# Optimization experiments

Measured on AMD Instinct MI355X. Metric: run time of the kernel, lower is better.

The kernel has to match this reference:

```python
import jax, jax.numpy as jnp
import numpy as np

B, S, D, H, F = 4, 2048, 256, 8, 2  # batch, seq, input_size, heads, mlp factor
EPS = 1e-5


def _ln(x, g, b):
    m = jnp.mean(x, axis=-1, keepdims=True)
    v = jnp.var(x, axis=-1, keepdims=True)
    return (x - m) / jnp.sqrt(v + EPS) * g + b


def setup_inputs() -> dict:
    key = jax.random.key(0)
    ks = jax.random.split(key, 12)
    s = 1.0 / np.sqrt(D)
    return {
        "X":  jax.random.normal(ks[0], (B, S, D), jnp.float32),
        # Wide attention: each of H heads has full [D,D] Q/K/V projections (no bias)
        "Wq": jax.random.uniform(ks[1], (H, D, D), jnp.float32, -s, s),
        "Wk": jax.random.uniform(ks[2], (H, D, D), jnp.float32, -s, s),
        "Wv": jax.random.uniform(ks[3], (H, D, D), jnp.float32, -s, s),
        "Wz": jax.random.uniform(ks[4], (H * D, D), jnp.float32, -1.0 / np.sqrt(H * D), 1.0 / np.sqrt(H * D)),
        "bz": jnp.zeros((D,), jnp.float32),
        "W1": jax.random.uniform(ks[5], (D, F * D), jnp.float32, -s, s),
        "b1": jnp.zeros((F * D,), jnp.float32),
        "W2": jax.random.uniform(ks[6], (F * D, D), jnp.float32, -1.0 / np.sqrt(F * D), 1.0 / np.sqrt(F * D)),
        "b2": jnp.zeros((D,), jnp.float32),
        "g1": jnp.ones((D,), jnp.float32),
        "be1": jnp.zeros((D,), jnp.float32),
        "g2": jnp.ones((D,), jnp.float32),
        "be2": jnp.zeros((D,), jnp.float32),
    }


def reference(X, Wq, Wk, Wv, Wz, bz, W1, b1, W2, b2, g1, be1, g2, be2):
    scale = D ** (-0.25)  # applied to both q and k as in the source
    q = jnp.einsum('bsd,hde->hbse', X, Wq) * scale   # [H,B,S,D]
    k = jnp.einsum('btd,hde->hbte', X, Wk) * scale
    v = jnp.einsum('btd,hde->hbte', X, Wv)
    attn = jax.nn.softmax(jnp.einsum('hbse,hbte->hbst', q, k), axis=-1)  # [H,B,S,S]
    zh = jnp.einsum('hbst,hbte->hbse', attn, v)       # [H,B,S,D]
    # concat heads along feature dim (head order matters for Wz)
    zcat = jnp.transpose(zh, (1, 2, 0, 3)).reshape(B, S, H * D)
    z = zcat @ Wz + bz
    z = _ln(z + X, g1, be1)                            # dropout p=0 -> identity
    z_ff = jnp.maximum(z @ W1 + b1, 0.0) @ W2 + b2
    z = _ln(z_ff + z, g2, be2)
    attn_mean = jnp.mean(attn, axis=0)                 # [B,S,S]
    return z, attn_mean
```

## Files before the change

### kernel.cpp

```cpp
#include <hip/hip_runtime.h>
#include <cstdint>
#include <cstddef>

#define B_  4
#define S_  2048
#define D_  256
#define H_  8
#define FD_ 512
#define N_  (B_*S_)
#define HD_ (H_*D_)
#define EPS 1e-5f

typedef __attribute__((ext_vector_type(8))) short bf16x8;
typedef __attribute__((ext_vector_type(8))) unsigned short u16x8;
typedef __attribute__((ext_vector_type(4))) float f32x4;

__device__ __forceinline__ unsigned short f2bf(float f) {
  union { float f; unsigned u; } x; x.f = f;
  unsigned u = x.u;
  return (unsigned short)((u + 0x7FFFu + ((u >> 16) & 1u)) >> 16);
}
__device__ __forceinline__ float bf2f(unsigned short h) {
  union { unsigned u; float f; } x; x.u = ((unsigned)h) << 16; return x.f;
}

__device__ __forceinline__ void glds16(const void* gptr, void* ldsptr) {
  __builtin_amdgcn_global_load_lds(
      (__attribute__((address_space(1))) void*)gptr,
      (__attribute__((address_space(3))) void*)ldsptr,
      16, 0, 0);
}

__device__ __forceinline__ int sw32(int row, int u) {
  return (row*32 + ((u & 24) | ((u & 7) ^ (row & 7)))) * 8;
}
__device__ __forceinline__ int sw16(int row, int u) {
  return (row*16 + ((u & 8) | ((u & 7) ^ (row & 7)))) * 8;
}

__global__ __launch_bounds__(256) void prep_fat_kernel(
    const float* __restrict__ X, unsigned short* __restrict__ Xb,
    const float* __restrict__ Wq, const float* __restrict__ Wk,
    const float* __restrict__ Wv, unsigned short* __restrict__ Wt,
    const float* __restrict__ Wz, unsigned short* __restrict__ Wzt,
    const float* __restrict__ W1, unsigned short* __restrict__ W1t,
    const float* __restrict__ W2, unsigned short* __restrict__ W2t)
{
  __shared__ float tile[64][65];
  const int tid = threadIdx.x;
  const int bid = blockIdx.x;

  if (bid < 1024) {
    const size_t i8 = ((size_t)bid * 256 + tid) * 8;
    float4 a = *(const float4*)&X[i8];
    float4 b = *(const float4*)&X[i8 + 4];
    u16x8 o;
    o[0]=f2bf(a.x); o[1]=f2bf(a.y); o[2]=f2bf(a.z); o[3]=f2bf(a.w);
    o[4]=f2bf(b.x); o[5]=f2bf(b.y); o[6]=f2bf(b.z); o[7]=f2bf(b.w);
    *(u16x8*)&Xb[i8] = o;
    return;
  }

  const float* src;
  unsigned short* dst_base;
  int R, C;
  float scale = 1.0f;
  int d0, e0;
  bool is_prepw = false;
  int wsel = 0;

  if (bid < 1408) {
    int idx = bid - 1024;
    d0 = (idx & 3) * 64;
    e0 = ((idx >> 2) & 3) * 64;
    wsel = idx >> 4;
    if (wsel < 8)       { src = Wq + (size_t)wsel*D_*D_;      scale = 0.25f; }
    else if (wsel < 16) { src = Wk + (size_t)(wsel-8)*D_*D_;  scale = 0.25f; }
    else                { src = Wv + (size_t)(wsel-16)*D_*D_; scale = 1.0f;  }
    R = D_; C = D_;
    dst_base = Wt;
    is_prepw = true;
  } else if (bid < 1536) {
    int idx = bid - 1408;
    d0 = (idx & 31) * 64;
    e0 = (idx >> 5) * 64;
    src = Wz; dst_base = Wzt; R = HD_; C = D_;
  } else if (bid < 1568) {
    int idx = bid - 1536;
    d0 = (idx & 3) * 64;
    e0 = (idx >> 2) * 64;
    src = W1; dst_base = W1t; R = D_; C = FD_;
  } else {
    int idx = bid - 1568;
    d0 = (idx & 7) * 64;
    e0 = (idx >> 3) * 64;
    src = W2; dst_base = W2t; R = FD_; C = D_;
  }

  {
    int r = tid >> 2, c16 = (tid & 3) * 16;
    const float* s = src + (size_t)(d0 + r)*C + e0 + c16;
    #pragma unroll
    for (int u = 0; u < 4; ++u) *(float4*)&tile[r][c16 + u*4] = *(const float4*)(s + u*4);
  }
  __syncthreads();
  {
    int cr = tid >> 2, rc = (tid & 3) * 16;
    u16x8 o0, o1;
    #pragma unroll
    for (int j = 0; j < 8; ++j) {
      o0[j] = f2bf(tile[rc + j][cr] * scale);
      o1[j] = f2bf(tile[rc + 8 + j][cr] * scale);
    }
    unsigned short* d;
    if (is_prepw)
      d = dst_base + ((size_t)wsel*D_ + e0 + cr)*D_ + d0 + rc;
    else
      d = dst_base + (size_t)(e0 + cr)*R + d0 + rc;
    *(u16x8*)(d)     = o0;
    *(u16x8*)(d + 8) = o1;
  }
}

__global__ __launch_bounds__(256) void qkv_kernel(
    const unsigned short* __restrict__ Xb, const unsigned short* __restrict__ Wt,
    unsigned short* __restrict__ q, unsigned short* __restrict__ k,
    unsigned short* __restrict__ vT)
{
  __shared__ unsigned short Xt[64*32*8];
  __shared__ unsigned short Wtile[64*32*8];
  const int tid = threadIdx.x;
  const int w4 = tid >> 6, lane = tid & 63;
  const int c = lane & 15, qd = lane >> 4;
  const int n0 = blockIdx.x * 64;
  const int e0 = blockIdx.y * 64;
  const int w  = blockIdx.z;

  {
    const char* xg = (const char*)Xb + (size_t)n0*512;
    const char* wg = (const char*)Wt + ((size_t)w*D_ + e0)*512;
    #pragma unroll
    for (int i = 0; i < 8; ++i) {
      int g = w4*8 + i;
      int r = 2*g + (lane >> 5);
      int su = lane & 31;
      int u = (su & 24) | ((su & 7) ^ (r & 7));
      glds16(xg + (size_t)r*512 + u*16, &Xt[g*512]);
      glds16(wg + (size_t)r*512 + u*16, &Wtile[g*512]);
    }
  }
  __syncthreads();

  f32x4 sc[4];
  #pragma unroll
  for (int nc = 0; nc < 4; ++nc) sc[nc] = (f32x4){0.f,0.f,0.f,0.f};
  #pragma unroll
  for (int ks = 0; ks < 8; ++ks) {
    bf16x8 xa = *(const bf16x8*)&Xt[sw32(16*w4 + c, ks*4 + qd)];
    #pragma unroll
    for (int nc = 0; nc < 4; ++nc) {
      bf16x8 bf = *(const bf16x8*)&Wtile[sw32(nc*16 + c, ks*4 + qd)];
      sc[nc] = __builtin_amdgcn_mfma_f32_16x16x32_bf16(xa, bf, sc[nc], 0, 0, 0);
    }
  }

  if (w < 16) {
    unsigned short* obase = (w < 8) ? (q + (size_t)w*N_*D_)
                                    : (k + (size_t)(w-8)*N_*D_);
    #pragma unroll
    for (int nc = 0; nc < 4; ++nc)
      #pragma unroll
      for (int r = 0; r < 4; ++r)
        obase[(size_t)(n0 + 16*w4 + qd*4 + r)*D_ + e0 + nc*16 + c] = f2bf(sc[nc][r]);
  } else {
    const int h = w - 16;
    const int b = n0 >> 11;
    const int t0 = n0 & (S_ - 1);
    unsigned short (*tile)[72] = (unsigned short (*)[72])Xt;
    __syncthreads();
    #pragma unroll
    for (int nc = 0; nc < 4; ++nc)
      #pragma unroll
      for (int r = 0; r < 4; ++r)
        tile[16*w4 + qd*4 + r][nc*16 + c] = f2bf(sc[nc][r]);
    __syncthreads();
    {
      int er = tid >> 2, tt = (tid & 3) * 16;
      u16x8 o0, o1;
      #pragma unroll
      for (int j = 0; j < 8; ++j) { o0[j] = tile[tt+j][er]; o1[j] = tile[tt+8+j][er]; }
      unsigned short* dst = vT + ((size_t)(h*4 + b)*D_ + e0 + er)*S_ + t0 + tt;
      *(u16x8*)(dst)     = o0;
      *(u16x8*)(dst + 8) = o1;
    }
  }
}

__global__ __launch_bounds__(256, 2) void attn_ol_kernel(
    const unsigned short* __restrict__ qb, const unsigned short* __restrict__ kb,
    const unsigned short* __restrict__ vT, unsigned short* __restrict__ zcatb,
    float* __restrict__ Lws)
{
  __shared__ unsigned short Kt[2][32*32*8];
  __shared__ unsigned short Vt[2][16*544];
  const int tid = threadIdx.x;
  const int w = tid >> 6, lane = tid & 63;
  const int c = lane & 15, qd = lane >> 4;
  const int wg = blockIdx.x;
  const int xcd = wg & 7;
  const int slot = wg >> 3;
  const int j = slot & 15;
  const int gg = slot >> 4;
  const int g = gg*8 + xcd;
  const int h = g >> 2, b = g & 3;
  const int s0 = j * 128;

  const size_t qkbase = (size_t)h*N_*D_ + (size_t)b*S_*D_;

  bf16x8 qa[2][8];
  #pragma unroll
  for (int mi = 0; mi < 2; ++mi) {
    const unsigned short* qrow = qb + qkbase + (size_t)(s0 + 32*w + 16*mi + c)*D_ + qd*8;
    #pragma unroll
    for (int ks = 0; ks < 8; ++ks) qa[mi][ks] = *(const bf16x8*)(qrow + ks*32);
  }

  f32x4 o[2][16];
  #pragma unroll
  for (int mi = 0; mi < 2; ++mi)
    #pragma unroll
    for (int i = 0; i < 16; ++i) o[mi][i] = (f32x4){0.f,0.f,0.f,0.f};
  float Lp[2] = {0.f, 0.f};

  const char* kB = (const char*)(kb + qkbase);
  const char* vB = (const char*)(vT + (size_t)(h*4 + b)*D_*S_);

  #define STAGE_OL(kt_, bi_)                                                   \
    {                                                                          \
      _Pragma("unroll")                                                        \
      for (int i = 0; i < 4; ++i) {                                            \
        int gq = w*4 + i;                                                      \
        int r = 2*gq + (lane >> 5);                                            \
        int Lg = ((r >> 2) & 3)*8 + (r >> 4)*4 + (r & 3);                      \
        int su = lane & 31;                                                    \
        int u = (su & 24) | ((su & 7) ^ (r & 7));                              \
        glds16(kB + ((size_t)(kt_)*32 + Lg)*512 + u*16, &Kt[bi_][gq*512]);     \
      }                                                                        \
      _Pragma("unroll")                                                        \
      for (int i = 0; i < 4; ++i) {                                            \
        int gq = w*4 + i;                                                      \
        int e = gq*16 + (lane >> 2);                                           \
        int qv = (lane & 3) ^ ((lane >> 3) & 3);                               \
        glds16(vB + (size_t)e*4096 + (size_t)(kt_)*64 + qv*16, &Vt[bi_][gq*544]);\
      }                                                                        \
    }

  STAGE_OL(0, 0);

  for (int kt = 0; kt < 64; ++kt) {
    const int bi = kt & 1;
    __syncthreads();
    if (kt + 1 < 64) STAGE_OL(kt + 1, bi ^ 1);

    f32x4 sc[2][2];
    #pragma unroll
    for (int mi = 0; mi < 2; ++mi)
      #pragma unroll
      for (int nc = 0; nc < 2; ++nc) sc[mi][nc] = (f32x4){0.f,0.f,0.f,0.f};
    #pragma unroll
    for (int ks = 0; ks < 8; ++ks) {
      bf16x8 kf0 = *(const bf16x8*)&Kt[bi][sw32(c,      ks*4 + qd)];
      bf16x8 kf1 = *(const bf16x8*)&Kt[bi][sw32(16 + c, ks*4 + qd)];
      #pragma unroll
      for (int mi = 0; mi < 2; ++mi) {
        sc[mi][0] = __builtin_amdgcn_mfma_f32_16x16x32_bf16(kf0, qa[mi][ks], sc[mi][0], 0, 0, 0);
        sc[mi][1] = __builtin_amdgcn_mfma_f32_16x16x32_bf16(kf1, qa[mi][ks], sc[mi][1], 0, 0, 0);
      }
    }
    bf16x8 pa[2];
    #pragma unroll
    for (int mi = 0; mi < 2; ++mi) {
      float ex[2][4];
      #pragma unroll
      for (int nc = 0; nc < 2; ++nc)
        #pragma unroll
        for (int r = 0; r < 4; ++r) {
          float p = __expf(sc[mi][nc][r]);
          ex[nc][r] = p;
          Lp[mi] += p;
        }
      union { unsigned u[4]; bf16x8 v; } cv;
      asm("v_cvt_pk_bf16_f32 %0, %1, %2" : "=v"(cv.u[0]) : "v"(ex[0][0]), "v"(ex[0][1]));
      asm("v_cvt_pk_bf16_f32 %0, %1, %2" : "=v"(cv.u[1]) : "v"(ex[0][2]), "v"(ex[0][3]));
      asm("v_cvt_pk_bf16_f32 %0, %1, %2" : "=v"(cv.u[2]) : "v"(ex[1][0]), "v"(ex[1][1]));
      asm("v_cvt_pk_bf16_f32 %0, %1, %2" : "=v"(cv.u[3]) : "v"(ex[1][2]), "v"(ex[1][3]));
      pa[mi] = cv.v;
    }
    #pragma unroll
    for (int ec = 0; ec < 16; ++ec) {
      bf16x8 vf = *(const bf16x8*)&Vt[bi][ec*544 + c*32 + (qd ^ ((c >> 1) & 3))*8];
      o[0][ec] = __builtin_amdgcn_mfma_f32_16x16x32_bf16(pa[0], vf, o[0][ec], 0, 0, 0);
      o[1][ec] = __builtin_amdgcn_mfma_f32_16x16x32_bf16(pa[1], vf, o[1][ec], 0, 0, 0);
    }
  }

  #pragma unroll
  for (int mi = 0; mi < 2; ++mi) {
    float L = Lp[mi];
    L += __shfl_xor(L, 16);
    L += __shfl_xor(L, 32);
    if (qd == 0)
      Lws[(size_t)h*N_ + b*S_ + s0 + 32*w + 16*mi + c] = L;
    float il[4];
    #pragma unroll
    for (int r = 0; r < 4; ++r)
      il[r] = 1.0f / __shfl(L, (lane & 48) | (qd*4 + r));
    #pragma unroll
    for (int ec = 0; ec < 16; ++ec)
      #pragma unroll
      for (int r = 0; r < 4; ++r)
        zcatb[(size_t)(b*S_ + s0 + 32*w + 16*mi + qd*4 + r)*HD_ + h*D_ + ec*16 + c] =
            f2bf(o[mi][ec][r] * il[r]);
  }
  #undef STAGE_OL
}

__global__ __launch_bounds__(256) void wz_ln1_kernel(
    const unsigned short* __restrict__ zcatb, const unsigned short* __restrict__ Wzt,
    const float* __restrict__ bz, const float* __restrict__ X,
    const float* __restrict__ g1, const float* __restrict__ be1,
    unsigned short* __restrict__ z1b)
{
  __shared__ unsigned short At[32*16*8];
  __shared__ unsigned short Wt2[256*16*8];
  __shared__ float redS[2][32], redQ[2][32];
  const int tid = threadIdx.x;
  const int w4 = tid >> 6, lane = tid & 63;
  const int c = lane & 15, qd = lane >> 4;
  const int n0 = blockIdx.x * 32;
  const int msub = w4 & 1, ehalf = w4 >> 1;

  f32x4 acc[8];
  #pragma unroll
  for (int nc = 0; nc < 8; ++nc) acc[nc] = (f32x4){0.f,0.f,0.f,0.f};

  for (int kc = 0; kc < 16; ++kc) {
    {
      const char* ab = (const char*)zcatb + (size_t)n0*4096 + (size_t)kc*256;
      #pragma unroll
      for (int i = 0; i < 2; ++i) {
        int g = w4*2 + i;
        int r = g*4 + (lane >> 4);
        int su = lane & 15;
        int u = (su & 8) | ((su & 7) ^ (r & 7));
        glds16(ab + (size_t)r*4096 + u*16, &At[g*512]);
      }
      const char* wb = (const char*)Wzt + (size_t)kc*256;
      #pragma unroll
      for (int i = 0; i < 16; ++i) {
        int g = w4*16 + i;
        int e = g*4 + (lane >> 4);
        int su = lane & 15;
        int u = (su & 8) | ((su & 7) ^ (e & 7));
        glds16(wb + (size_t)e*4096 + u*16, &Wt2[g*512]);
      }
    }
    __syncthreads();
    #pragma unroll
    for (int ks = 0; ks < 4; ++ks) {
      bf16x8 a = *(const bf16x8*)&At[sw16(msub*16 + c, ks*4 + qd)];
      #pragma unroll
      for (int nc = 0; nc < 8; ++nc) {
        bf16x8 bv = *(const bf16x8*)&Wt2[sw16(ehalf*128 + nc*16 + c, ks*4 + qd)];
        acc[nc] = __builtin_amdgcn_mfma_f32_16x16x32_bf16(a, bv, acc[nc], 0, 0, 0);
      }
    }
    __syncthreads();
  }

  float vals[8][4];
  float sum_[4] = {0.f,0.f,0.f,0.f}, sq_[4] = {0.f,0.f,0.f,0.f};
  #pragma unroll
  for (int nc = 0; nc < 8; ++nc) {
    int e = ehalf*128 + nc*16 + c;
    #pragma unroll
    for (int r = 0; r < 4; ++r) {
      int n = n0 + msub*16 + qd*4 + r;
      float v = acc[nc][r] + bz[e] + X[(size_t)n*D_ + e];
      vals[nc][r] = v;
      sum_[r] += v; sq_[r] += v*v;
    }
  }
  #pragma unroll
  for (int off = 1; off < 16; off <<= 1) {
    #pragma unroll
    for (int r = 0; r < 4; ++r) {
      sum_[r] += __shfl_xor(sum_[r], off);
      sq_[r]  += __shfl_xor(sq_[r],  off);
    }
  }
  if (c == 0) {
    #pragma unroll
    for (int r = 0; r < 4; ++r) {
      redS[ehalf][msub*16 + qd*4 + r] = sum_[r];
      redQ[ehalf][msub*16 + qd*4 + r] = sq_[r];
    }
  }
  __syncthreads();
  #pragma unroll
  for (int r = 0; r < 4; ++r) {
    int lr = msub*16 + qd*4 + r;
    float Sv = redS[0][lr] + redS[1][lr];
    float Qv = redQ[0][lr] + redQ[1][lr];
    float mean = Sv * (1.0f/D_);
    float var  = Qv * (1.0f/D_) - mean*mean;
    float rstd = rsqrtf(var + EPS);
    int n = n0 + lr;
    #pragma unroll
    for (int nc = 0; nc < 8; ++nc) {
      int e = ehalf*128 + nc*16 + c;
      z1b[(size_t)n*D_ + e] = f2bf((vals[nc][r] - mean)*rstd*g1[e] + be1[e]);
    }
  }
}

__global__ __launch_bounds__(256, 2) void attn_mean_mlp1_kernel(
    const unsigned short* __restrict__ qb, const unsigned short* __restrict__ kb,
    const float* __restrict__ Lws, float* __restrict__ out_attn,
    const unsigned short* __restrict__ z1b, const unsigned short* __restrict__ W1t,
    const float* __restrict__ b1, unsigned short* __restrict__ hbuf)
{
  __shared__ __align__(16) char smem[65536];
  const int tid = threadIdx.x;
  const int w = tid >> 6, lane = tid & 63;
  const int c = lane & 15, qd = lane >> 4;
  const int bid = blockIdx.x;

  if (bid < 2048) {
    unsigned short (*Kt)[64*32*8] = (unsigned short (*)[64*32*8])smem;
    const int xcd = bid & 7;
    const int slot = bid >> 3;
    const int j = slot & 15;
    const int ggg = slot >> 4;
    const int g = ggg*8 + xcd;
    const int b = g >> 5;
    const int t0 = (g & 31) * 64;
    const int s0 = j * 128;

    float am[2][4][4] = {};

    #define STAGE_AM(h_, bi_)                                                  \
      {                                                                        \
        const char* kB = (const char*)(kb + (size_t)(h_)*N_*D_ + (size_t)b*S_*D_);\
        _Pragma("unroll")                                                      \
        for (int i = 0; i < 8; ++i) {                                          \
          int gq = w*8 + i;                                                    \
          int r = 2*gq + (lane >> 5);                                          \
          int su = lane & 31;                                                  \
          int u = (su & 24) | ((su & 7) ^ (r & 7));                            \
          glds16(kB + ((size_t)t0 + r)*512 + u*16, &Kt[bi_][gq*512]);          \
        }                                                                      \
      }

    STAGE_AM(0, 0);

    bf16x8 qa[2][8];
    #pragma unroll
    for (int mi = 0; mi < 2; ++mi) {
      const unsigned short* qrow = qb + (size_t)b*S_*D_ + (size_t)(s0 + 32*w + 16*mi + c)*D_ + qd*8;
      #pragma unroll
      for (int ks = 0; ks < 8; ++ks) qa[mi][ks] = *(const bf16x8*)(qrow + ks*32);
    }

    for (int h = 0; h < 8; ++h) {
      const int bi = h & 1;
      __syncthreads();
      if (h + 1 < 8) STAGE_AM(h + 1, bi ^ 1);

      float il[2][4];
      #pragma unroll
      for (int mi = 0; mi < 2; ++mi)
        #pragma unroll
        for (int r = 0; r < 4; ++r)
          il[mi][r] = 0.125f / Lws[(size_t)h*N_ + b*S_ + s0 + 32*w + 16*mi + qd*4 + r];

      bf16x8 qn[2][8];
      if (h + 1 < 8) {
        const size_t basen = (size_t)(h+1)*N_*D_ + (size_t)b*S_*D_;
        #pragma unroll
        for (int mi = 0; mi < 2; ++mi) {
          const unsigned short* qrow = qb + basen + (size_t)(s0 + 32*w + 16*mi + c)*D_ + qd*8;
          #pragma unroll
          for (int ks = 0; ks < 8; ++ks) qn[mi][ks] = *(const bf16x8*)(qrow + ks*32);
        }
      }

      f32x4 sc[2][4];
      #pragma unroll
      for (int mi = 0; mi < 2; ++mi)
        #pragma unroll
        for (int nc = 0; nc < 4; ++nc) sc[mi][nc] = (f32x4){0.f,0.f,0.f,0.f};
      #pragma unroll
      for (int ks = 0; ks < 8; ++ks) {
        #pragma unroll
        for (int nc = 0; nc < 4; ++nc) {
          bf16x8 kf = *(const bf16x8*)&Kt[bi][sw32(nc*16 + c, ks*4 + qd)];
          sc[0][nc] = __builtin_amdgcn_mfma_f32_16x16x32_bf16(qa[0][ks], kf, sc[0][nc], 0, 0, 0);
          sc[1][nc] = __builtin_amdgcn_mfma_f32_16x16x32_bf16(qa[1][ks], kf, sc[1][nc], 0, 0, 0);
        }
      }
      #pragma unroll
      for (int mi = 0; mi < 2; ++mi)
        #pragma unroll
        for (int nc = 0; nc < 4; ++nc)
          #pragma unroll
          for (int r = 0; r < 4; ++r)
            am[mi][nc][r] += __expf(sc[mi][nc][r]) * il[mi][r];

      if (h + 1 < 8) {
        #pragma unroll
        for (int mi = 0; mi < 2; ++mi)
          #pragma unroll
          for (int ks = 0; ks < 8; ++ks) qa[mi][ks] = qn[mi][ks];
      }
    }
    #pragma unroll
    for (int mi = 0; mi < 2; ++mi)
      #pragma unroll
      for (int nc = 0; nc < 4; ++nc)
        #pragma unroll
        for (int r = 0; r < 4; ++r)
          out_attn[(size_t)(b*S_ + s0 + 32*w + 16*mi + qd*4 + r)*S_ + t0 + nc*16 + c] =
              am[mi][nc][r];
    #undef STAGE_AM
  } else {
    unsigned short* At = (unsigned short*)smem;
    unsigned short* Bt = (unsigned short*)(smem + 32768);
    const int idx = bid - 2048;
    const int n0 = (idx & 127) * 64;
    const int f0 = (idx >> 7) * 64;
    const int w4 = w;

    {
      const char* ag = (const char*)z1b + (size_t)n0*512;
      const char* bg = (const char*)W1t + (size_t)f0*512;
      #pragma unroll
      for (int i = 0; i < 8; ++i) {
        int g = w4*8 + i;
        int r = 2*g + (lane >> 5);
        int su = lane & 31;
        int u = (su & 24) | ((su & 7) ^ (r & 7));
        glds16(ag + (size_t)r*512 + u*16, &At[g*512]);
        glds16(bg + (size_t)r*512 + u*16, &Bt[g*512]);
      }
    }
    __syncthreads();

    f32x4 sc[4];
    #pragma unroll
    for (int nc = 0; nc < 4; ++nc) sc[nc] = (f32x4){0.f,0.f,0.f,0.f};
    #pragma unroll
    for (int ks = 0; ks < 8; ++ks) {
      bf16x8 xa = *(const bf16x8*)&At[sw32(16*w4 + c, ks*4 + qd)];
      #pragma unroll
      for (int nc = 0; nc < 4; ++nc) {
        bf16x8 bf = *(const bf16x8*)&Bt[sw32(nc*16 + c, ks*4 + qd)];
        sc[nc] = __builtin_amdgcn_mfma_f32_16x16x32_bf16(xa, bf, sc[nc], 0, 0, 0);
      }
    }
    #pragma unroll
    for (int nc = 0; nc < 4; ++nc) {
      int f = f0 + nc*16 + c;
      float bias = b1[f];
      #pragma unroll
      for (int r = 0; r < 4; ++r)
        hbuf[(size_t)(n0 + 16*w4 + qd*4 + r)*FD_ + f] = f2bf(fmaxf(sc[nc][r] + bias, 0.f));
    }
  }
}

__global__ __launch_bounds__(256) void mlp2_kernel(
    const unsigned short* __restrict__ hbuf, const unsigned short* __restrict__ W2t,
    const float* __restrict__ b2, const unsigned short* __restrict__ z1b,
    const float* __restrict__ g2, const float* __restrict__ be2,
    float* __restrict__ out)
{
  __shared__ unsigned short At[32*16*8];
  __shared__ unsigned short Wt2[256*16*8];
  __shared__ float redS[2][32], redQ[2][32];
  const int tid = threadIdx.x;
  const int w4 = tid >> 6, lane = tid & 63;
  const int c = lane & 15, qd = lane >> 4;
  const int n0 = blockIdx.x * 32;
  const int msub = w4 & 1, ehalf = w4 >> 1;

  f32x4 acc[8];
  #pragma unroll
  for (int nc = 0; nc < 8; ++nc) acc[nc] = (f32x4){0.f,0.f,0.f,0.f};

  for (int kc = 0; kc < 4; ++kc) {
    {
      const char* ab = (const char*)hbuf + (size_t)n0*1024 + (size_t)kc*256;
      #pragma unroll
      for (int i = 0; i < 2; ++i) {
        int g = w4*2 + i;
        int r = g*4 + (lane >> 4);
        int su = lane & 15;
        int u = (su & 8) | ((su & 7) ^ (r & 7));
        glds16(ab + (size_t)r*1024 + u*16, &At[g*512]);
      }
      const char* wb = (const char*)W2t + (size_t)kc*256;
      #pragma unroll
      for (int i = 0; i < 16; ++i) {
        int g = w4*16 + i;
        int e = g*4 + (lane >> 4);
        int su = lane & 15;
        int u = (su & 8) | ((su & 7) ^ (e & 7));
        glds16(wb + (size_t)e*1024 + u*16, &Wt2[g*512]);
      }
    }
    __syncthreads();
    #pragma unroll
    for (int ks = 0; ks < 4; ++ks) {
      bf16x8 a = *(const bf16x8*)&At[sw16(msub*16 + c, ks*4 + qd)];
      #pragma unroll
      for (int nc = 0; nc < 8; ++nc) {
        bf16x8 bv = *(const bf16x8*)&Wt2[sw16(ehalf*128 + nc*16 + c, ks*4 + qd)];
        acc[nc] = __builtin_amdgcn_mfma_f32_16x16x32_bf16(a, bv, acc[nc], 0, 0, 0);
      }
    }
    __syncthreads();
  }

  float vals[8][4];
  float sum_[4] = {0.f,0.f,0.f,0.f}, sq_[4] = {0.f,0.f,0.f,0.f};
  #pragma unroll
  for (int nc = 0; nc < 8; ++nc) {
    int e = ehalf*128 + nc*16 + c;
    #pragma unroll
    for (int r = 0; r < 4; ++r) {
      int n = n0 + msub*16 + qd*4 + r;
      float v = acc[nc][r] + b2[e] + bf2f(z1b[(size_t)n*D_ + e]);
      vals[nc][r] = v;
      sum_[r] += v; sq_[r] += v*v;
    }
  }
  #pragma unroll
  for (int off = 1; off < 16; off <<= 1) {
    #pragma unroll
    for (int r = 0; r < 4; ++r) {
      sum_[r] += __shfl_xor(sum_[r], off);
      sq_[r]  += __shfl_xor(sq_[r],  off);
    }
  }
  if (c == 0) {
    #pragma unroll
    for (int r = 0; r < 4; ++r) {
      redS[ehalf][msub*16 + qd*4 + r] = sum_[r];
      redQ[ehalf][msub*16 + qd*4 + r] = sq_[r];
    }
  }
  __syncthreads();
  #pragma unroll
  for (int r = 0; r < 4; ++r) {
    int lr = msub*16 + qd*4 + r;
    float Sv = redS[0][lr] + redS[1][lr];
    float Qv = redQ[0][lr] + redQ[1][lr];
    float mean = Sv * (1.0f/D_);
    float var  = Qv * (1.0f/D_) - mean*mean;
    float rstd = rsqrtf(var + EPS);
    int n = n0 + lr;
    #pragma unroll
    for (int nc = 0; nc < 8; ++nc) {
      int e = ehalf*128 + nc*16 + c;
      out[(size_t)n*D_ + e] = (vals[nc][r] - mean)*rstd*g2[e] + be2[e];
    }
  }
}

extern "C" void kernel_launch(void* const* d_in, const int* in_sizes, int n_in,
                              void* d_out, int out_size, void* d_ws, size_t ws_size,
                              hipStream_t stream)
{
  (void)in_sizes; (void)n_in; (void)out_size; (void)ws_size;
  const float* X   = (const float*)d_in[0];
  const float* Wq  = (const float*)d_in[1];
  const float* Wk  = (const float*)d_in[2];
  const float* Wv  = (const float*)d_in[3];
  const float* Wz  = (const float*)d_in[4];
  const float* bz  = (const float*)d_in[5];
  const float* W1  = (const float*)d_in[6];
  const float* b1  = (const float*)d_in[7];
  const float* W2  = (const float*)d_in[8];
  const float* b2  = (const float*)d_in[9];
  const float* g1  = (const float*)d_in[10];
  const float* be1 = (const float*)d_in[11];
  const float* g2  = (const float*)d_in[12];
  const float* be2 = (const float*)d_in[13];

  char* p = (char*)d_ws;
  unsigned short* Xbb  = (unsigned short*)p; p += (size_t)N_*D_*2;
  unsigned short* Wtb  = (unsigned short*)p; p += (size_t)24*D_*D_*2;
  unsigned short* Wztb = (unsigned short*)p; p += (size_t)D_*HD_*2;
  unsigned short* W1tb = (unsigned short*)p; p += (size_t)FD_*D_*2;
  unsigned short* W2tb = (unsigned short*)p; p += (size_t)D_*FD_*2;
  unsigned short* qbuf = (unsigned short*)p; p += (size_t)H_*N_*D_*2;
  unsigned short* kbuf = (unsigned short*)p; p += (size_t)H_*N_*D_*2;
  unsigned short* vbuf = (unsigned short*)p; p += (size_t)H_*N_*D_*2;
  unsigned short* vTb  = (unsigned short*)p; p += (size_t)H_*N_*D_*2;
  float* Lws   = (float*)p; p += (size_t)H_*N_*4;
  unsigned short* zcatb = (unsigned short*)p; p += (size_t)N_*HD_*2;
  unsigned short* z1b   = (unsigned short*)p; p += (size_t)N_*D_*2;
  unsigned short* hbuf  = (unsigned short*)p;
  (void)vbuf;

  float* out_z    = (float*)d_out;
  float* out_attn = out_z + (size_t)N_*D_;

  prep_fat_kernel<<<1600, 256, 0, stream>>>(
      X, Xbb, Wq, Wk, Wv, Wtb, Wz, Wztb, W1, W1tb, W2, W2tb);

  dim3 gA(N_/64, D_/64, 24);
  qkv_kernel<<<gA, 256, 0, stream>>>(Xbb, Wtb, qbuf, kbuf, vTb);

  attn_ol_kernel<<<512, 256, 0, stream>>>(qbuf, kbuf, vTb, zcatb, Lws);

  wz_ln1_kernel<<<N_/32, 256, 0, stream>>>(zcatb, Wztb, bz, X, g1, be1, z1b);

  attn_mean_mlp1_kernel<<<3072, 256, 0, stream>>>(
      qbuf, kbuf, Lws, out_attn, z1b, W1tb, b1, hbuf);

  mlp2_kernel<<<N_/32, 256, 0, stream>>>(hbuf, W2tb, b2, z1b, g2, be2, out_z);
}
```

Baseline: 504.7 us.

## Split attention-mean work across two fused kernels to overlap Wz+LN1 and MLP1

The attention-mean computation is split into two halves over query blocks. The first half now runs in the same launch as the Wz projection plus LayerNorm1, and the second half in the same launch as the MLP1 GEMM. This is meant to hide the small, low-occupancy Wz/LN1 kernel behind independent attention-mean work and balance the two launches. The Wz/LN1 branch now uses a larger shared allocation (about 74KB) under launch bounds of 2 blocks per CU, which can reduce occupancy for the attention-mean blocks in that launch.

```diff
diff --git a/kernel.cpp b/kernel.cpp
--- a/kernel.cpp
+++ b/kernel.cpp
@@ -325,123 +325,27 @@
   #undef STAGE_OL
 }
 
-__global__ __launch_bounds__(256) void wz_ln1_kernel(
+#define FATSMEM (73728 + 512)
+__global__ __launch_bounds__(256, 2) void fat_a_kernel(
+    const unsigned short* __restrict__ qb, const unsigned short* __restrict__ kb,
+    const float* __restrict__ Lws, float* __restrict__ out_attn,
     const unsigned short* __restrict__ zcatb, const unsigned short* __restrict__ Wzt,
     const float* __restrict__ bz, const float* __restrict__ X,
     const float* __restrict__ g1, const float* __restrict__ be1,
     unsigned short* __restrict__ z1b)
 {
-  __shared__ unsigned short At[32*16*8];
-  __shared__ unsigned short Wt2[256*16*8];
-  __shared__ float redS[2][32], redQ[2][32];
-  const int tid = threadIdx.x;
-  const int w4 = tid >> 6, lane = tid & 63;
-  const int c = lane & 15, qd = lane >> 4;
-  const int n0 = blockIdx.x * 32;
-  const int msub = w4 & 1, ehalf = w4 >> 1;
-
-  f32x4 acc[8];
-  #pragma unroll
-  for (int nc = 0; nc < 8; ++nc) acc[nc] = (f32x4){0.f,0.f,0.f,0.f};
-
-  for (int kc = 0; kc < 16; ++kc) {
-    {
-      const char* ab = (const char*)zcatb + (size_t)n0*4096 + (size_t)kc*256;
-      #pragma unroll
-      for (int i = 0; i < 2; ++i) {
-        int g = w4*2 + i;
-        int r = g*4 + (lane >> 4);
-        int su = lane & 15;
-        int u = (su & 8) | ((su & 7) ^ (r & 7));
-        glds16(ab + (size_t)r*4096 + u*16, &At[g*512]);
-      }
-      const char* wb = (const char*)Wzt + (size_t)kc*256;
-      #pragma unroll
-      for (int i = 0; i < 16; ++i) {
-        int g = w4*16 + i;
-        int e = g*4 + (lane >> 4);
-        int su = lane & 15;
-        int u = (su & 8) | ((su & 7) ^ (e & 7));
-        glds16(wb + (size_t)e*4096 + u*16, &Wt2[g*512]);
-      }
-    }
-    __syncthreads();
-    #pragma unroll
-    for (int ks = 0; ks < 4; ++ks) {
-      bf16x8 a = *(const bf16x8*)&At[sw16(msub*16 + c, ks*4 + qd)];
-      #pragma unroll
-      for (int nc = 0; nc < 8; ++nc) {
-        bf16x8 bv = *(const bf16x8*)&Wt2[sw16(ehalf*128 + nc*16 + c, ks*4 + qd)];
-        acc[nc] = __builtin_amdgcn_mfma_f32_16x16x32_bf16(a, bv, acc[nc], 0, 0, 0);
-      }
-    }
-    __syncthreads();
-  }
-
-  float vals[8][4];
-  float sum_[4] = {0.f,0.f,0.f,0.f}, sq_[4] = {0.f,0.f,0.f,0.f};
-  #pragma unroll
-  for (int nc = 0; nc < 8; ++nc) {
-    int e = ehalf*128 + nc*16 + c;
-    #pragma unroll
-    for (int r = 0; r < 4; ++r) {
-      int n = n0 + msub*16 + qd*4 + r;
-      float v = acc[nc][r] + bz[e] + X[(size_t)n*D_ + e];
-      vals[nc][r] = v;
-      sum_[r] += v; sq_[r] += v*v;
-    }
-  }
-  #pragma unroll
-  for (int off = 1; off < 16; off <<= 1) {
-    #pragma unroll
-    for (int r = 0; r < 4; ++r) {
-      sum_[r] += __shfl_xor(sum_[r], off);
-      sq_[r]  += __shfl_xor(sq_[r],  off);
-    }
-  }
-  if (c == 0) {
-    #pragma unroll
-    for (int r = 0; r < 4; ++r) {
-      redS[ehalf][msub*16 + qd*4 + r] = sum_[r];
-      redQ[ehalf][msub*16 + qd*4 + r] = sq_[r];
-    }
-  }
-  __syncthreads();
-  #pragma unroll
-  for (int r = 0; r < 4; ++r) {
-    int lr = msub*16 + qd*4 + r;
-    float Sv = redS[0][lr] + redS[1][lr];
-    float Qv = redQ[0][lr] + redQ[1][lr];
-    float mean = Sv * (1.0f/D_);
-    float var  = Qv * (1.0f/D_) - mean*mean;
-    float rstd = rsqrtf(var + EPS);
-    int n = n0 + lr;
-    #pragma unroll
-    for (int nc = 0; nc < 8; ++nc) {
-      int e = ehalf*128 + nc*16 + c;
-      z1b[(size_t)n*D_ + e] = f2bf((vals[nc][r] - mean)*rstd*g1[e] + be1[e]);
-    }
-  }
-}
-
-__global__ __launch_bounds__(256, 2) void attn_mean_mlp1_kernel(
-    const unsigned short* __restrict__ qb, const unsigned short* __restrict__ kb,
-    const float* __restrict__ Lws, float* __restrict__ out_attn,
-    const unsigned short* __restrict__ z1b, const unsigned short* __restrict__ W1t,
-    const float* __restrict__ b1, unsigned short* __restrict__ hbuf)
-{
-  __shared__ __align__(16) char smem[65536];
+  __shared__ __align__(16) char smem[FATSMEM];
   const int tid = threadIdx.x;
   const int w = tid >> 6, lane = tid & 63;
   const int c = lane & 15, qd = lane >> 4;
   const int bid = blockIdx.x;
 
-  if (bid < 2048) {
+  if (bid < 1024) {
     unsigned short (*Kt)[64*32*8] = (unsigned short (*)[64*32*8])smem;
     const int xcd = bid & 7;
     const int slot = bid >> 3;
-    const int j = slot & 15;
-    const int ggg = slot >> 4;
+    const int j = slot & 7;
+    const int ggg = slot >> 3;
     const int g = ggg*8 + xcd;
     const int b = g >> 5;
     const int t0 = (g & 31) * 64;
@@ -534,9 +438,212 @@
               am[mi][nc][r];
     #undef STAGE_AM
   } else {
+    unsigned short* At  = (unsigned short*)smem;
+    unsigned short* Wt2 = (unsigned short*)(smem + 8192);
+    float (*redS)[32] = (float (*)[32])(smem + 73728);
+    float (*redQ)[32] = (float (*)[32])(smem + 73728 + 256);
+    const int n0 = (bid - 1024) * 32;
+    const int w4 = w;
+    const int msub = w4 & 1, ehalf = w4 >> 1;
+
+    f32x4 acc[8];
+    #pragma unroll
+    for (int nc = 0; nc < 8; ++nc) acc[nc] = (f32x4){0.f,0.f,0.f,0.f};
+
+    for (int kc = 0; kc < 16; ++kc) {
+      {
+        const char* ab = (const char*)zcatb + (size_t)n0*4096 + (size_t)kc*256;
+        #pragma unroll
+        for (int i = 0; i < 2; ++i) {
+          int g = w4*2 + i;
+          int r = g*4 + (lane >> 4);
+          int su = lane & 15;
+          int u = (su & 8) | ((su & 7) ^ (r & 7));
+          glds16(ab + (size_t)r*4096 + u*16, &At[g*512]);
+        }
+        const char* wb = (const char*)Wzt + (size_t)kc*256;
+        #pragma unroll
+        for (int i = 0; i < 16; ++i) {
+          int g = w4*16 + i;
+          int e = g*4 + (lane >> 4);
+          int su = lane & 15;
+          int u = (su & 8) | ((su & 7) ^ (e & 7));
+          glds16(wb + (size_t)e*4096 + u*16, &Wt2[g*512]);
+        }
+      }
+      __syncthreads();
+      #pragma unroll
+      for (int ks = 0; ks < 4; ++ks) {
+        bf16x8 a = *(const bf16x8*)&At[sw16(msub*16 + c, ks*4 + qd)];
+        #pragma unroll
+        for (int nc = 0; nc < 8; ++nc) {
+          bf16x8 bv = *(const bf16x8*)&Wt2[sw16(ehalf*128 + nc*16 + c, ks*4 + qd)];
+          acc[nc] = __builtin_amdgcn_mfma_f32_16x16x32_bf16(a, bv, acc[nc], 0, 0, 0);
+        }
+      }
+      __syncthreads();
+    }
+
+    float vals[8][4];
+    float sum_[4] = {0.f,0.f,0.f,0.f}, sq_[4] = {0.f,0.f,0.f,0.f};
+    #pragma unroll
+    for (int nc = 0; nc < 8; ++nc) {
+      int e = ehalf*128 + nc*16 + c;
+      #pragma unroll
+      for (int r = 0; r < 4; ++r) {
+        int n = n0 + msub*16 + qd*4 + r;
+        float v = acc[nc][r] + bz[e] + X[(size_t)n*D_ + e];
+        vals[nc][r] = v;
+        sum_[r] += v; sq_[r] += v*v;
+      }
+    }
+    #pragma unroll
+    for (int off = 1; off < 16; off <<= 1) {
+      #pragma unroll
+      for (int r = 0; r < 4; ++r) {
+        sum_[r] += __shfl_xor(sum_[r], off);
+        sq_[r]  += __shfl_xor(sq_[r],  off);
+      }
+    }
+    if (c == 0) {
+      #pragma unroll
+      for (int r = 0; r < 4; ++r) {
+        redS[ehalf][msub*16 + qd*4 + r] = sum_[r];
+        redQ[ehalf][msub*16 + qd*4 + r] = sq_[r];
+      }
+    }
+    __syncthreads();
+    #pragma unroll
+    for (int r = 0; r < 4; ++r) {
+      int lr = msub*16 + qd*4 + r;
+      float Sv = redS[0][lr] + redS[1][lr];
+      float Qv = redQ[0][lr] + redQ[1][lr];
+      float mean = Sv * (1.0f/D_);
+      float var  = Qv * (1.0f/D_) - mean*mean;
+      float rstd = rsqrtf(var + EPS);
+      int n = n0 + lr;
+      #pragma unroll
+      for (int nc = 0; nc < 8; ++nc) {
+        int e = ehalf*128 + nc*16 + c;
+        z1b[(size_t)n*D_ + e] = f2bf((vals[nc][r] - mean)*rstd*g1[e] + be1[e]);
+      }
+    }
+  }
+}
+
+__global__ __launch_bounds__(256, 2) void fat_b_kernel(
+    const unsigned short* __restrict__ qb, const unsigned short* __restrict__ kb,
+    const float* __restrict__ Lws, float* __restrict__ out_attn,
+    const unsigned short* __restrict__ z1b, const unsigned short* __restrict__ W1t,
+    const float* __restrict__ b1, unsigned short* __restrict__ hbuf)
+{
+  __shared__ __align__(16) char smem[65536];
+  const int tid = threadIdx.x;
+  const int w = tid >> 6, lane = tid & 63;
+  const int c = lane & 15, qd = lane >> 4;
+  const int bid = blockIdx.x;
+
+  if (bid < 1024) {
+    unsigned short (*Kt)[64*32*8] = (unsigned short (*)[64*32*8])smem;
+    const int xcd = bid & 7;
+    const int slot = bid >> 3;
+    const int j = 8 + (slot & 7);
+    const int ggg = slot >> 3;
+    const int g = ggg*8 + xcd;
+    const int b = g >> 5;
+    const int t0 = (g & 31) * 64;
+    const int s0 = j * 128;
+
+    float am[2][4][4] = {};
+
+    #define STAGE_AM(h_, bi_)                                                  \
+      {                                                                        \
+        const char* kB = (const char*)(kb + (size_t)(h_)*N_*D_ + (size_t)b*S_*D_);\
+        _Pragma("unroll")                                                      \
+        for (int i = 0; i < 8; ++i) {                                          \
+          int gq = w*8 + i;                                                    \
+          int r = 2*gq + (lane >> 5);                                          \
+          int su = lane & 31;                                                  \
+          int u = (su & 24) | ((su & 7) ^ (r & 7));                            \
+          glds16(kB + ((size_t)t0 + r)*512 + u*16, &Kt[bi_][gq*512]);          \
+        }                                                                      \
+      }
+
+    STAGE_AM(0, 0);
+
+    bf16x8 qa[2][8];
+    #pragma unroll
+    for (int mi = 0; mi < 2; ++mi) {
+      const unsigned short* qrow = qb + (size_t)b*S_*D_ + (size_t)(s0 + 32*w + 16*mi + c)*D_ + qd*8;
+      #pragma unroll
+      for (int ks = 0; ks < 8; ++ks) qa[mi][ks] = *(const bf16x8*)(qrow + ks*32);
+    }
+
+    for (int h = 0; h < 8; ++h) {
+      const int bi = h & 1;
+      __syncthreads();
+      if (h + 1 < 8) STAGE_AM(h + 1, bi ^ 1);
+
+      float il[2][4];
+      #pragma unroll
+      for (int mi = 0; mi < 2; ++mi)
+        #pragma unroll
+        for (int r = 0; r < 4; ++r)
+          il[mi][r] = 0.125f / Lws[(size_t)h*N_ + b*S_ + s0 + 32*w + 16*mi + qd*4 + r];
+
+      bf16x8 qn[2][8];
+      if (h + 1 < 8) {
+        const size_t basen = (size_t)(h+1)*N_*D_ + (size_t)b*S_*D_;
+        #pragma unroll
+        for (int mi = 0; mi < 2; ++mi) {
+          const unsigned short* qrow = qb + basen + (size_t)(s0 + 32*w + 16*mi + c)*D_ + qd*8;
+          #pragma unroll
+          for (int ks = 0; ks < 8; ++ks) qn[mi][ks] = *(const bf16x8*)(qrow + ks*32);
+        }
+      }
+
+      f32x4 sc[2][4];
+      #pragma unroll
+      for (int mi = 0; mi < 2; ++mi)
+        #pragma unroll
+        for (int nc = 0; nc < 4; ++nc) sc[mi][nc] = (f32x4){0.f,0.f,0.f,0.f};
+      #pragma unroll
+      for (int ks = 0; ks < 8; ++ks) {
+        #pragma unroll
+        for (int nc = 0; nc < 4; ++nc) {
+          bf16x8 kf = *(const bf16x8*)&Kt[bi][sw32(nc*16 + c, ks*4 + qd)];
+          sc[0][nc] = __builtin_amdgcn_mfma_f32_16x16x32_bf16(qa[0][ks], kf, sc[0][nc], 0, 0, 0);
+          sc[1][nc] = __builtin_amdgcn_mfma_f32_16x16x32_bf16(qa[1][ks], kf, sc[1][nc], 0, 0, 0);
+        }
+      }
+      #pragma unroll
+      for (int mi = 0; mi < 2; ++mi)
+        #pragma unroll
+        for (int nc = 0; nc < 4; ++nc)
+          #pragma unroll
+          for (int r = 0; r < 4; ++r)
+            am[mi][nc][r] += __expf(sc[mi][nc][r]) * il[mi][r];
+
+      if (h + 1 < 8) {
+        #pragma unroll
+        for (int mi = 0; mi < 2; ++mi)
+          #pragma unroll
+          for (int ks = 0; ks < 8; ++ks) qa[mi][ks] = qn[mi][ks];
+      }
+    }
+    #pragma unroll
+    for (int mi = 0; mi < 2; ++mi)
+      #pragma unroll
+      for (int nc = 0; nc < 4; ++nc)
+        #pragma unroll
+        for (int r = 0; r < 4; ++r)
+          out_attn[(size_t)(b*S_ + s0 + 32*w + 16*mi + qd*4 + r)*S_ + t0 + nc*16 + c] =
+              am[mi][nc][r];
+    #undef STAGE_AM
+  } else {
     unsigned short* At = (unsigned short*)smem;
     unsigned short* Bt = (unsigned short*)(smem + 32768);
-    const int idx = bid - 2048;
+    const int idx = bid - 1024;
     const int n0 = (idx & 127) * 64;
     const int f0 = (idx >> 7) * 64;
     const int w4 = w;
@@ -725,9 +832,10 @@
 
   attn_ol_kernel<<<512, 256, 0, stream>>>(qbuf, kbuf, vTb, zcatb, Lws);
 
-  wz_ln1_kernel<<<N_/32, 256, 0, stream>>>(zcatb, Wztb, bz, X, g1, be1, z1b);
-
-  attn_mean_mlp1_kernel<<<3072, 256, 0, stream>>>(
+  fat_a_kernel<<<1280, 256, 0, stream>>>(
+      qbuf, kbuf, Lws, out_attn, zcatb, Wztb, bz, X, g1, be1, z1b);
+
+  fat_b_kernel<<<2048, 256, 0, stream>>>(
       qbuf, kbuf, Lws, out_attn, z1b, W1tb, b1, hbuf);
 
   mlp2_kernel<<<N_/32, 256, 0, stream>>>(hbuf, W2tb, b2, z1b, g2, be2, out_z);
```

New measurement: 503.9 us. Within noise of the previous version (-0.2%).
